# Optimization experiments

Measured on AMD Instinct MI355X. Metric: run time of the kernel, lower is better.

The kernel has to match this reference:

```python
import jax, jax.numpy as jnp
import numpy as np
import math

B, L, M = 8, 1024, 1024
H, D, DK, DFF = 16, 1024, 64, 4096
EPS = 1e-5


def _ln(x, g, b):
    mu = jnp.mean(x, axis=-1, keepdims=True)
    var = jnp.mean((x - mu) ** 2, axis=-1, keepdims=True)
    return (x - mu) * jax.lax.rsqrt(var + EPS) * g + b


def _mha(x, kv, Wq, bq, Wk, bk, Wv, bv, Wo, bo, masked):
    # x: [B,Lq,D], kv: [B,Lk,D]; per-head weights stacked: Wq [H,D,DK], bq [H,DK]
    Q = jnp.einsum('bld,hdk->bhlk', x, Wq) + bq[None, :, None, :]
    K = jnp.einsum('bld,hdk->bhlk', kv, Wk) + bk[None, :, None, :]
    V = jnp.einsum('bld,hdk->bhlk', kv, Wv) + bv[None, :, None, :]
    scores = jnp.einsum('bhqk,bhmk->bhqm', Q, K) / math.sqrt(DK)
    p = jax.nn.softmax(scores, axis=-1)
    if masked:
        # faithful to source: mask applied AFTER softmax (multiply by tril ones)
        Lq = x.shape[1]
        tril = jnp.tril(jnp.ones((Lq, kv.shape[1]), dtype=p.dtype))
        p = p * tril
    z = jnp.einsum('bhqm,bhmk->bhqk', p, V)  # [B,H,Lq,DK]
    z = jnp.transpose(z, (0, 2, 1, 3)).reshape(x.shape[0], x.shape[1], H * DK)
    return z @ Wo + bo


def _forward(x, enc, Wq1, bq1, Wk1, bk1, Wv1, bv1, Wo1, bo1,
             Wq2, bq2, Wk2, bk2, Wv2, bv2, Wo2, bo2,
             W1, b1, W2, b2, g1, be1, g2, be2, g3, be3):
    z = _mha(x, x, Wq1, bq1, Wk1, bk1, Wv1, bv1, Wo1, bo1, masked=True)
    x = _ln(z + x, g1, be1)
    z = _mha(x, enc, Wq2, bq2, Wk2, bk2, Wv2, bv2, Wo2, bo2, masked=False)
    x = _ln(z + x, g2, be2)
    # Conv1d(k=1) pair == per-token MLP: relu(x @ W1 + b1) @ W2 + b2
    y = jax.nn.relu(x @ W1 + b1) @ W2 + b2
    return _ln(y + x, g3, be3)


def setup_inputs() -> dict:
    key = jax.random.key(0)
    ks = jax.random.split(key, 16)
    s = 0.02
    return {
        'x': jax.random.normal(ks[0], (B, L, D), jnp.float32),
        'enc': jax.random.normal(ks[1], (B, M, D), jnp.float32),
        'Wq1': jax.random.normal(ks[2], (H, D, DK), jnp.float32) * s,
        'bq1': jnp.zeros((H, DK), jnp.float32),
        'Wk1': jax.random.normal(ks[3], (H, D, DK), jnp.float32) * s,
        'bk1': jnp.zeros((H, DK), jnp.float32),
        'Wv1': jax.random.normal(ks[4], (H, D, DK), jnp.float32) * s,
        'bv1': jnp.zeros((H, DK), jnp.float32),
        'Wo1': jax.random.normal(ks[5], (H * DK, D), jnp.float32) * s,
        'bo1': jnp.zeros((D,), jnp.float32),
        'Wq2': jax.random.normal(ks[6], (H, D, DK), jnp.float32) * s,
        'bq2': jnp.zeros((H, DK), jnp.float32),
        'Wk2': jax.random.normal(ks[7], (H, D, DK), jnp.float32) * s,
        'bk2': jnp.zeros((H, DK), jnp.float32),
        'Wv2': jax.random.normal(ks[8], (H, D, DK), jnp.float32) * s,
        'bv2': jnp.zeros((H, DK), jnp.float32),
        'Wo2': jax.random.normal(ks[9], (H * DK, D), jnp.float32) * s,
        'bo2': jnp.zeros((D,), jnp.float32),
        'W1': jax.random.normal(ks[10], (D, DFF), jnp.float32) * s,
        'b1': jnp.zeros((DFF,), jnp.float32),
        'W2': jax.random.normal(ks[11], (DFF, D), jnp.float32) * s,
        'b2': jnp.zeros((D,), jnp.float32),
        'g1': jnp.ones((D,), jnp.float32), 'be1': jnp.zeros((D,), jnp.float32),
        'g2': jnp.ones((D,), jnp.float32), 'be2': jnp.zeros((D,), jnp.float32),
        'g3': jnp.ones((D,), jnp.float32), 'be3': jnp.zeros((D,), jnp.float32),
    }


def reference(x, enc, Wq1, bq1, Wk1, bk1, Wv1, bv1, Wo1, bo1,
              Wq2, bq2, Wk2, bk2, Wv2, bv2, Wo2, bo2,
              W1, b1, W2, b2, g1, be1, g2, be2, g3, be3):
    return _forward(x, enc, Wq1, bq1, Wk1, bk1, Wv1, bv1, Wo1, bo1,
                    Wq2, bq2, Wk2, bk2, Wv2, bv2, Wo2, bo2,
                    W1, b1, W2, b2, g1, be1, g2, be2, g3, be3)
```

## Files before the change

kernel.cpp:

```cpp
#include <hip/hip_runtime.h>
#include <hip/hip_bf16.h>

typedef __bf16 bf16;
typedef __bf16 bf16x8 __attribute__((ext_vector_type(8)));
typedef __bf16 bf16x4v __attribute__((ext_vector_type(4)));
typedef float f32x4 __attribute__((ext_vector_type(4)));

#define DEV static __device__ __forceinline__

DEV void gll16(const void* g, void* l) {
  __builtin_amdgcn_global_load_lds((__attribute__((address_space(1))) void*)g,
                                   (__attribute__((address_space(3))) void*)l,
                                   16, 0, 0);
}

DEV bf16 tobf(float f) { return (bf16)f; }

__global__ void cast_f2b_kernel(const float* __restrict__ in, bf16* __restrict__ out, int n4) {
  int i = blockIdx.x * 256 + threadIdx.x;
  if (i < n4) {
    const float4 v = ((const float4*)in)[i];
    bf16x4v o;
    o[0] = tobf(v.x); o[1] = tobf(v.y); o[2] = tobf(v.z); o[3] = tobf(v.w);
    ((bf16x4v*)out)[i] = o;
  }
}

__global__ __launch_bounds__(256)
void tpack_kernel(const float* __restrict__ in, bf16* __restrict__ out,
                  int K, int N, int in_hs, int out_hs, float scale) {
  __shared__ float tile[32][33];
  const int k0 = blockIdx.x << 5, n0 = blockIdx.y << 5;
  const float* ip = in + (size_t)blockIdx.z * in_hs;
  bf16* op = out + (size_t)blockIdx.z * out_hs;
  const int tx = threadIdx.x & 31, ty = threadIdx.x >> 5;
#pragma unroll
  for (int r = 0; r < 4; ++r)
    tile[ty * 4 + r][tx] = ip[(size_t)(k0 + ty * 4 + r) * N + n0 + tx];
  __syncthreads();
#pragma unroll
  for (int r = 0; r < 4; ++r)
    op[(size_t)(n0 + ty * 4 + r) * K + k0 + tx] = tobf(tile[tx][ty * 4 + r] * scale);
}

__global__ void bscale_kernel(const float* __restrict__ in, float* __restrict__ out, int n, float s) {
  int i = blockIdx.x * 256 + threadIdx.x;
  if (i < n) out[i] = in[i] * s;
}

template<int EPI>
__global__ __launch_bounds__(256, 2)
void gemm_bt(const bf16* __restrict__ A, const bf16* __restrict__ W,
             const float* __restrict__ bias, const float* __restrict__ resid,
             void* __restrict__ outv, int M, int N, int K) {
  __shared__ bf16 sA[2][128 * 64];
  __shared__ bf16 sB[2][128 * 64];
  const int nbx = N >> 7;
  const int nwg = (M >> 7) * nbx;
  int bid = (int)blockIdx.x;
  bid = (bid & 7) * (nwg >> 3) + (bid >> 3);
  const int tm = bid / nbx, tn = bid - tm * nbx;
  const int tid = threadIdx.x;
  const int lane = tid & 63;
  const int w = tid >> 6;
  const int wm = (w >> 1) << 6, wn = (w & 1) << 6;
  const int l15 = lane & 15, l4 = lane >> 4;

  int srow[4], scol[4];
#pragma unroll
  for (int j = 0; j < 4; ++j) {
    int g = tid + (j << 8);
    srow[j] = g >> 3;
    scol[j] = ((g & 7) ^ (srow[j] & 7)) << 3;
  }
  const bf16* Abase = A + (size_t)(tm * 128) * K;
  const bf16* Bbase = W + (size_t)(tn * 128) * K;

  f32x4 acc[4][4] = {};
  const int nt = K >> 6;
  int cur = 0;

  auto stage = [&](int buf, int t) {
    const int kb = t << 6;
#pragma unroll
    for (int j = 0; j < 4; ++j) {
      int g = tid + (j << 8);
      gll16(Abase + (size_t)srow[j] * K + kb + scol[j], &sA[buf][g << 3]);
    }
#pragma unroll
    for (int j = 0; j < 4; ++j) {
      int g = tid + (j << 8);
      gll16(Bbase + (size_t)srow[j] * K + kb + scol[j], &sB[buf][g << 3]);
    }
  };

  stage(0, 0);
  __syncthreads();

  for (int t = 0; t < nt; ++t) {
    if (t + 1 < nt) stage(cur ^ 1, t + 1);
    bf16x8 af[4][2], bfm[4][2];
#pragma unroll
    for (int mi = 0; mi < 4; ++mi)
#pragma unroll
      for (int kk = 0; kk < 2; ++kk) {
        int r = wm + (mi << 4) + l15;
        int off = (r << 7) + (kk << 6) + (l4 << 4);
        off ^= (r & 7) << 4;
        af[mi][kk] = *(const bf16x8*)((const char*)sA[cur] + off);
      }
#pragma unroll
    for (int ni = 0; ni < 4; ++ni)
#pragma unroll
      for (int kk = 0; kk < 2; ++kk) {
        int r = wn + (ni << 4) + l15;
        int off = (r << 7) + (kk << 6) + (l4 << 4);
        off ^= (r & 7) << 4;
        bfm[ni][kk] = *(const bf16x8*)((const char*)sB[cur] + off);
      }
#pragma unroll
    for (int mi = 0; mi < 4; ++mi)
#pragma unroll
      for (int ni = 0; ni < 4; ++ni)
#pragma unroll
        for (int kk = 0; kk < 2; ++kk)
          acc[mi][ni] = __builtin_amdgcn_mfma_f32_16x16x32_bf16(af[mi][kk], bfm[ni][kk],
                                                                acc[mi][ni], 0, 0, 0);
    __syncthreads();
    cur ^= 1;
  }

  const int row0 = tm * 128 + wm + (l4 << 2);
  const int col0 = tn * 128 + wn + l15;
#pragma unroll
  for (int ni = 0; ni < 4; ++ni) {
    const int col = col0 + (ni << 4);
    const float bv = bias ? bias[col] : 0.f;
#pragma unroll
    for (int mi = 0; mi < 4; ++mi) {
      const int rr = row0 + (mi << 4);
      f32x4 v = acc[mi][ni];
      if (EPI == 0) {
        bf16* out = (bf16*)outv;
#pragma unroll
        for (int r = 0; r < 4; ++r) out[(size_t)(rr + r) * N + col] = tobf(v[r] + bv);
      } else if (EPI == 1) {
        float* out = (float*)outv;
#pragma unroll
        for (int r = 0; r < 4; ++r) {
          size_t idx = (size_t)(rr + r) * N + col;
          out[idx] = v[r] + bv + resid[idx];
        }
      } else if (EPI == 2) {
        bf16* out = (bf16*)outv;
#pragma unroll
        for (int r = 0; r < 4; ++r) out[(size_t)(rr + r) * N + col] = tobf(fmaxf(v[r] + bv, 0.f));
      } else {
        bf16* out = (bf16*)outv;
        const int bb = rr >> 10, l0 = rr & 1023;
        const int hh = col >> 6, dk = col & 63;
        bf16x4v pk;
#pragma unroll
        for (int r = 0; r < 4; ++r) pk[r] = tobf(v[r] + bv);
        *(bf16x4v*)(out + ((size_t)((bb * 16 + hh) * 64 + dk) << 10) + l0) = pk;
      }
    }
  }
}

template<bool MASKED>
__global__ __launch_bounds__(256, 3)
void attn_kernel(const bf16* __restrict__ Qp, const bf16* __restrict__ Kp,
                 const bf16* __restrict__ Vt, bf16* __restrict__ Z) {
  __shared__ bf16 sK[2][64 * 64];
  __shared__ bf16 sV[2][64 * 64];
  __shared__ bf16 sP[4][32 * 72];
  const int Lk = 1024;
  const int d = blockIdx.x;
  const int bh = d & 127, qb = d >> 7;
  const int b = bh >> 4, h = bh & 15;
  const int q0 = qb << 7;
  const int tid = threadIdx.x, lane = tid & 63, w = tid >> 6;
  const int l15 = lane & 15, l4 = lane >> 4;

  const bf16* Qb = Qp + ((size_t)(b * 1024 + q0 + w * 32)) * 1024 + h * 64;
  bf16x8 qf[2][2];
#pragma unroll
  for (int mi = 0; mi < 2; ++mi)
#pragma unroll
    for (int kk = 0; kk < 2; ++kk)
      qf[mi][kk] = *(const bf16x8*)(Qb + (size_t)((mi << 4) + l15) * 1024 + (kk << 5) + (l4 << 3));

  f32x4 o[4][2] = {};
  float Mr[2][4], Lr[2][4];
#pragma unroll
  for (int mi = 0; mi < 2; ++mi)
#pragma unroll
    for (int r = 0; r < 4; ++r) { Mr[mi][r] = -1e30f; Lr[mi][r] = 0.f; }

  const bf16* Kb = Kp + ((size_t)b * Lk) * 1024 + h * 64;
  const bf16* Vb = Vt + ((size_t)(b * 16 + h)) * 64 * Lk;

  auto stage = [&](int buf, int t, bool withV) {
    const int kv0 = t << 6;
#pragma unroll
    for (int j = 0; j < 2; ++j) {
      int g = tid + (j << 8);
      int r = g >> 3;
      int sc = ((g & 7) ^ (r & 7)) << 3;
      gll16(Kb + (size_t)(kv0 + r) * 1024 + sc, &sK[buf][g << 3]);
      if (withV) gll16(Vb + (size_t)r * Lk + kv0 + sc, &sV[buf][g << 3]);
    }
  };
  auto needPV = [&](int t) -> bool { return !MASKED || ((t << 6) < q0 + 128); };

  const int NT = Lk >> 6;
  stage(0, 0, true);
  __syncthreads();
  int cur = 0;

  for (int t = 0; t < NT; ++t) {
    if (t + 1 < NT) stage(cur ^ 1, t + 1, needPV(t + 1));
    const int kv0 = t << 6;

    bf16x8 kf[4][2];
#pragma unroll
    for (int n = 0; n < 4; ++n)
#pragma unroll
      for (int kk = 0; kk < 2; ++kk) {
        int r = (n << 4) + l15;
        int off = (r << 7) + (kk << 6) + (l4 << 4);
        off ^= (r & 7) << 4;
        kf[n][kk] = *(const bf16x8*)((const char*)sK[cur] + off);
      }
    f32x4 s[4][2] = {};
#pragma unroll
    for (int n = 0; n < 4; ++n)
#pragma unroll
      for (int mi = 0; mi < 2; ++mi)
#pragma unroll
        for (int kk = 0; kk < 2; ++kk)
          s[n][mi] = __builtin_amdgcn_mfma_f32_16x16x32_bf16(qf[mi][kk], kf[n][kk],
                                                             s[n][mi], 0, 0, 0);

#pragma unroll
    for (int mi = 0; mi < 2; ++mi)
#pragma unroll
      for (int r = 0; r < 4; ++r) {
        float tmx = fmaxf(fmaxf(s[0][mi][r], s[1][mi][r]), fmaxf(s[2][mi][r], s[3][mi][r]));
#pragma unroll
        for (int dd = 1; dd < 16; dd <<= 1) tmx = fmaxf(tmx, __shfl_xor(tmx, dd, 64));
        const float Mn = fmaxf(Mr[mi][r], tmx);
        const float al = __expf(Mr[mi][r] - Mn);
        float rs = 0.f;
#pragma unroll
        for (int n = 0; n < 4; ++n) {
          float p = __expf(s[n][mi][r] - Mn);
          s[n][mi][r] = p;
          rs += p;
        }
#pragma unroll
        for (int dd = 1; dd < 16; dd <<= 1) rs += __shfl_xor(rs, dd, 64);
        Lr[mi][r] = Lr[mi][r] * al + rs;
        Mr[mi][r] = Mn;
#pragma unroll
        for (int nd = 0; nd < 4; ++nd) o[nd][mi][r] *= al;
      }

    if (needPV(t)) {
#pragma unroll
      for (int n = 0; n < 4; ++n)
#pragma unroll
        for (int mi = 0; mi < 2; ++mi)
#pragma unroll
          for (int r = 0; r < 4; ++r) {
            float v = s[n][mi][r];
            if (MASKED) {
              int cg = kv0 + (n << 4) + l15;
              int rg = q0 + (w << 5) + (mi << 4) + (l4 << 2) + r;
              if (cg > rg) v = 0.f;
            }
            sP[w][((mi << 4) + (l4 << 2) + r) * 72 + (n << 4) + l15] = tobf(v);
          }

      bf16x8 vf[4][2], pa[2][2];
#pragma unroll
      for (int nd = 0; nd < 4; ++nd)
#pragma unroll
        for (int kk = 0; kk < 2; ++kk) {
          int r = (nd << 4) + l15;
          int off = (r << 7) + (kk << 6) + (l4 << 4);
          off ^= (r & 7) << 4;
          vf[nd][kk] = *(const bf16x8*)((const char*)sV[cur] + off);
        }
#pragma unroll
      for (int mi = 0; mi < 2; ++mi)
#pragma unroll
        for (int kk = 0; kk < 2; ++kk)
          pa[mi][kk] = *(const bf16x8*)((const char*)sP[w] +
                                        ((mi << 4) + l15) * 144 + (kk << 6) + (l4 << 4));
#pragma unroll
      for (int nd = 0; nd < 4; ++nd)
#pragma unroll
        for (int mi = 0; mi < 2; ++mi)
#pragma unroll
          for (int kk = 0; kk < 2; ++kk)
            o[nd][mi] = __builtin_amdgcn_mfma_f32_16x16x32_bf16(pa[mi][kk], vf[nd][kk],
                                                                o[nd][mi], 0, 0, 0);
    }
    __syncthreads();
    cur ^= 1;
  }

  float inv[2][4];
#pragma unroll
  for (int mi = 0; mi < 2; ++mi)
#pragma unroll
    for (int r = 0; r < 4; ++r) inv[mi][r] = 1.f / Lr[mi][r];
  bf16* Zb = Z + ((size_t)(b * 1024 + q0 + w * 32)) * 1024 + h * 64;
#pragma unroll
  for (int nd = 0; nd < 4; ++nd)
#pragma unroll
    for (int mi = 0; mi < 2; ++mi)
#pragma unroll
      for (int r = 0; r < 4; ++r)
        Zb[(size_t)((mi << 4) + (l4 << 2) + r) * 1024 + (nd << 4) + l15] =
            tobf(o[nd][mi][r] * inv[mi][r]);
}

__global__ __launch_bounds__(256)
void ln_kernel(const float* __restrict__ in, const float* __restrict__ gw,
               const float* __restrict__ bw, float* __restrict__ outf,
               bf16* __restrict__ outb) {
  const int row = blockIdx.x, tid = threadIdx.x;
  const size_t base = (size_t)row << 10;
  const float4 v = *(const float4*)(in + base + tid * 4);
  float s = v.x + v.y + v.z + v.w;
  float ss = v.x * v.x + v.y * v.y + v.z * v.z + v.w * v.w;
#pragma unroll
  for (int d = 1; d < 64; d <<= 1) { s += __shfl_xor(s, d, 64); ss += __shfl_xor(ss, d, 64); }
  __shared__ float red[8];
  const int w = tid >> 6;
  if ((tid & 63) == 0) { red[w] = s; red[4 + w] = ss; }
  __syncthreads();
  s = red[0] + red[1] + red[2] + red[3];
  ss = red[4] + red[5] + red[6] + red[7];
  const float mu = s * (1.f / 1024.f);
  const float var = ss * (1.f / 1024.f) - mu * mu;
  const float rstd = rsqrtf(var + 1e-5f);
  const float4 g4 = *(const float4*)(gw + tid * 4);
  const float4 b4 = *(const float4*)(bw + tid * 4);
  const float o0 = (v.x - mu) * rstd * g4.x + b4.x;
  const float o1 = (v.y - mu) * rstd * g4.y + b4.y;
  const float o2 = (v.z - mu) * rstd * g4.z + b4.z;
  const float o3 = (v.w - mu) * rstd * g4.w + b4.w;
  if (outf) { float4 of; of.x = o0; of.y = o1; of.z = o2; of.w = o3;
              *(float4*)(outf + base + tid * 4) = of; }
  if (outb) { bf16x4v ob; ob[0] = tobf(o0); ob[1] = tobf(o1); ob[2] = tobf(o2); ob[3] = tobf(o3);
              *(bf16x4v*)(outb + base + tid * 4) = ob; }
}

extern "C" void kernel_launch(void* const* d_in, const int* in_sizes, int n_in,
                              void* d_out, int out_size, void* d_ws, size_t ws_size,
                              hipStream_t stream) {
  const float* x   = (const float*)d_in[0];
  const float* enc = (const float*)d_in[1];
  const float* Wq1 = (const float*)d_in[2];
  const float* bq1 = (const float*)d_in[3];
  const float* Wk1 = (const float*)d_in[4];
  const float* bk1 = (const float*)d_in[5];
  const float* Wv1 = (const float*)d_in[6];
  const float* bv1 = (const float*)d_in[7];
  const float* Wo1 = (const float*)d_in[8];
  const float* bo1 = (const float*)d_in[9];
  const float* Wq2 = (const float*)d_in[10];
  const float* bq2 = (const float*)d_in[11];
  const float* Wk2 = (const float*)d_in[12];
  const float* bk2 = (const float*)d_in[13];
  const float* Wv2 = (const float*)d_in[14];
  const float* bv2 = (const float*)d_in[15];
  const float* Wo2 = (const float*)d_in[16];
  const float* bo2 = (const float*)d_in[17];
  const float* W1  = (const float*)d_in[18];
  const float* b1  = (const float*)d_in[19];
  const float* W2  = (const float*)d_in[20];
  const float* b2  = (const float*)d_in[21];
  const float* g1  = (const float*)d_in[22];
  const float* be1 = (const float*)d_in[23];
  const float* g2  = (const float*)d_in[24];
  const float* be2 = (const float*)d_in[25];
  const float* g3  = (const float*)d_in[26];
  const float* be3 = (const float*)d_in[27];

  char* ws = (char*)d_ws;
  size_t off = 0;
  auto alloc = [&](size_t bytes) { char* p = ws + off; off += (bytes + 255) & ~(size_t)255; return p; };
  const size_t ACT = (size_t)8 * 1024 * 1024 * 2;
  const size_t WSQ = (size_t)1024 * 1024 * 2;

  bf16* xb    = (bf16*)alloc(ACT);
  bf16* encb  = (bf16*)alloc(ACT);
  bf16* Wq1t  = (bf16*)alloc(WSQ);
  bf16* Wk1t  = (bf16*)alloc(WSQ);
  bf16* Wv1t  = (bf16*)alloc(WSQ);
  bf16* Wq2t  = (bf16*)alloc(WSQ);
  bf16* Wk2t  = (bf16*)alloc(WSQ);
  bf16* Wv2t  = (bf16*)alloc(WSQ);
  bf16* Wo1t  = (bf16*)alloc(WSQ);
  bf16* Wo2t  = (bf16*)alloc(WSQ);
  bf16* W1t   = (bf16*)alloc((size_t)4096 * 1024 * 2);
  bf16* W2t   = (bf16*)alloc((size_t)4096 * 1024 * 2);
  float* sbq1 = (float*)alloc(4096);
  float* sbq2 = (float*)alloc(4096);
  char*  S    = alloc((size_t)64 * 1024 * 1024);
  float* rbuf = (float*)alloc((size_t)8 * 1024 * 1024 * 4);
  float* xnf  = (float*)alloc((size_t)8 * 1024 * 1024 * 4);
  bf16*  xnb  = (bf16*)alloc(ACT);

  bf16* q1   = (bf16*)(S);
  bf16* k1   = (bf16*)(S + ACT);
  bf16* vt1  = (bf16*)(S + 2 * ACT);
  bf16* z1   = (bf16*)(S + 3 * ACT);
  bf16* hbuf = (bf16*)S;

  dim3 b256(256);
  cast_f2b_kernel<<<8192, b256, 0, stream>>>(x, xb, 2097152);
  cast_f2b_kernel<<<8192, b256, 0, stream>>>(enc, encb, 2097152);
  tpack_kernel<<<dim3(32, 2, 16), b256, 0, stream>>>(Wq1, Wq1t, 1024, 64, 65536, 65536, 0.125f);
  tpack_kernel<<<dim3(32, 2, 16), b256, 0, stream>>>(Wk1, Wk1t, 1024, 64, 65536, 65536, 1.f);
  tpack_kernel<<<dim3(32, 2, 16), b256, 0, stream>>>(Wv1, Wv1t, 1024, 64, 65536, 65536, 1.f);
  tpack_kernel<<<dim3(32, 2, 16), b256, 0, stream>>>(Wq2, Wq2t, 1024, 64, 65536, 65536, 0.125f);
  tpack_kernel<<<dim3(32, 2, 16), b256, 0, stream>>>(Wk2, Wk2t, 1024, 64, 65536, 65536, 1.f);
  tpack_kernel<<<dim3(32, 2, 16), b256, 0, stream>>>(Wv2, Wv2t, 1024, 64, 65536, 65536, 1.f);
  tpack_kernel<<<dim3(32, 32, 1), b256, 0, stream>>>(Wo1, Wo1t, 1024, 1024, 0, 0, 1.f);
  tpack_kernel<<<dim3(32, 32, 1), b256, 0, stream>>>(Wo2, Wo2t, 1024, 1024, 0, 0, 1.f);
  tpack_kernel<<<dim3(32, 128, 1), b256, 0, stream>>>(W1, W1t, 1024, 4096, 0, 0, 1.f);
  tpack_kernel<<<dim3(128, 32, 1), b256, 0, stream>>>(W2, W2t, 4096, 1024, 0, 0, 1.f);
  bscale_kernel<<<4, b256, 0, stream>>>(bq1, sbq1, 1024, 0.125f);
  bscale_kernel<<<4, b256, 0, stream>>>(bq2, sbq2, 1024, 0.125f);

  gemm_bt<0><<<512, b256, 0, stream>>>(xb, Wq1t, sbq1, nullptr, q1, 8192, 1024, 1024);
  gemm_bt<0><<<512, b256, 0, stream>>>(xb, Wk1t, bk1, nullptr, k1, 8192, 1024, 1024);
  gemm_bt<3><<<512, b256, 0, stream>>>(xb, Wv1t, bv1, nullptr, vt1, 8192, 1024, 1024);
  attn_kernel<true><<<1024, b256, 0, stream>>>(q1, k1, vt1, z1);
  gemm_bt<1><<<512, b256, 0, stream>>>(z1, Wo1t, bo1, x, rbuf, 8192, 1024, 1024);
  ln_kernel<<<8192, b256, 0, stream>>>(rbuf, g1, be1, xnf, xnb);

  gemm_bt<0><<<512, b256, 0, stream>>>(xnb, Wq2t, sbq2, nullptr, q1, 8192, 1024, 1024);
  gemm_bt<0><<<512, b256, 0, stream>>>(encb, Wk2t, bk2, nullptr, k1, 8192, 1024, 1024);
  gemm_bt<3><<<512, b256, 0, stream>>>(encb, Wv2t, bv2, nullptr, vt1, 8192, 1024, 1024);
  attn_kernel<false><<<1024, b256, 0, stream>>>(q1, k1, vt1, z1);
  gemm_bt<1><<<512, b256, 0, stream>>>(z1, Wo2t, bo2, xnf, rbuf, 8192, 1024, 1024);
  ln_kernel<<<8192, b256, 0, stream>>>(rbuf, g2, be2, xnf, xnb);

  gemm_bt<2><<<2048, b256, 0, stream>>>(xnb, W1t, b1, nullptr, hbuf, 8192, 4096, 1024);
  gemm_bt<1><<<512, b256, 0, stream>>>(hbuf, W2t, b2, xnf, rbuf, 8192, 1024, 4096);
  ln_kernel<<<8192, b256, 0, stream>>>(rbuf, g3, be3, (float*)d_out, nullptr);
}
```

Measured before the change: 664.0 us.

## Compute transposed scores in attention and pass P via register shuffles

The attention kernel now computes S^T, with K as the A operand and Q as B, so that each lane holds the scores for one query row. The row max and sum then need only two cross-lane shuffles instead of four per value. The softmax probabilities are packed to bf16 with v_cvt_pk_bf16_f32 and moved into the PV MFMA operand layout with lane shuffles, which removes the per-wave LDS scratch buffer sP and its stores and loads. The exp becomes exp2 with log2(e) folded into the Q weight and bias scaling, the mask is applied only on tiles that need it, and launch bounds rise to 4 waves per SIMD. The gains could be offset by the added shuffles and by register pressure at the higher occupancy target.

```diff
diff --git a/kernel.cpp b/kernel.cpp
--- a/kernel.cpp
+++ b/kernel.cpp
@@ -5,6 +5,8 @@
 typedef __bf16 bf16x8 __attribute__((ext_vector_type(8)));
 typedef __bf16 bf16x4v __attribute__((ext_vector_type(4)));
 typedef float f32x4 __attribute__((ext_vector_type(4)));
+typedef unsigned int u32;
+typedef u32 u32x4 __attribute__((ext_vector_type(4)));
 
 #define DEV static __device__ __forceinline__
 
@@ -15,6 +17,12 @@
 }
 
 DEV bf16 tobf(float f) { return (bf16)f; }
+
+DEV u32 cvtpk(float lo, float hi) {
+  u32 r;
+  asm("v_cvt_pk_bf16_f32 %0, %1, %2" : "=v"(r) : "v"(lo), "v"(hi));
+  return r;
+}
 
 __global__ void cast_f2b_kernel(const float* __restrict__ in, bf16* __restrict__ out, int n4) {
   int i = blockIdx.x * 256 + threadIdx.x;
@@ -169,12 +177,11 @@
 }
 
 template<bool MASKED>
-__global__ __launch_bounds__(256, 3)
+__global__ __launch_bounds__(256, 4)
 void attn_kernel(const bf16* __restrict__ Qp, const bf16* __restrict__ Kp,
                  const bf16* __restrict__ Vt, bf16* __restrict__ Z) {
   __shared__ bf16 sK[2][64 * 64];
   __shared__ bf16 sV[2][64 * 64];
-  __shared__ bf16 sP[4][32 * 72];
   const int Lk = 1024;
   const int d = blockIdx.x;
   const int bh = d & 127, qb = d >> 7;
@@ -192,11 +199,7 @@
       qf[mi][kk] = *(const bf16x8*)(Qb + (size_t)((mi << 4) + l15) * 1024 + (kk << 5) + (l4 << 3));
 
   f32x4 o[4][2] = {};
-  float Mr[2][4], Lr[2][4];
-#pragma unroll
-  for (int mi = 0; mi < 2; ++mi)
-#pragma unroll
-    for (int r = 0; r < 4; ++r) { Mr[mi][r] = -1e30f; Lr[mi][r] = 0.f; }
+  float Mr[2] = {-1e30f, -1e30f}, Lr[2] = {0.f, 0.f};
 
   const bf16* Kb = Kp + ((size_t)b * Lk) * 1024 + h * 64;
   const bf16* Vb = Vt + ((size_t)(b * 16 + h)) * 64 * Lk;
@@ -223,90 +226,113 @@
     if (t + 1 < NT) stage(cur ^ 1, t + 1, needPV(t + 1));
     const int kv0 = t << 6;
 
-    bf16x8 kf[4][2];
-#pragma unroll
-    for (int n = 0; n < 4; ++n)
+    f32x4 s[4][2] = {};
+#pragma unroll
+    for (int n = 0; n < 4; ++n) {
+      bf16x8 kf[2];
 #pragma unroll
       for (int kk = 0; kk < 2; ++kk) {
         int r = (n << 4) + l15;
         int off = (r << 7) + (kk << 6) + (l4 << 4);
         off ^= (r & 7) << 4;
-        kf[n][kk] = *(const bf16x8*)((const char*)sK[cur] + off);
-      }
-    f32x4 s[4][2] = {};
-#pragma unroll
-    for (int n = 0; n < 4; ++n)
+        kf[kk] = *(const bf16x8*)((const char*)sK[cur] + off);
+      }
 #pragma unroll
       for (int mi = 0; mi < 2; ++mi)
 #pragma unroll
         for (int kk = 0; kk < 2; ++kk)
-          s[n][mi] = __builtin_amdgcn_mfma_f32_16x16x32_bf16(qf[mi][kk], kf[n][kk],
+          s[n][mi] = __builtin_amdgcn_mfma_f32_16x16x32_bf16(kf[kk], qf[mi][kk],
                                                              s[n][mi], 0, 0, 0);
-
-#pragma unroll
-    for (int mi = 0; mi < 2; ++mi)
-#pragma unroll
-      for (int r = 0; r < 4; ++r) {
-        float tmx = fmaxf(fmaxf(s[0][mi][r], s[1][mi][r]), fmaxf(s[2][mi][r], s[3][mi][r]));
-#pragma unroll
-        for (int dd = 1; dd < 16; dd <<= 1) tmx = fmaxf(tmx, __shfl_xor(tmx, dd, 64));
-        const float Mn = fmaxf(Mr[mi][r], tmx);
-        const float al = __expf(Mr[mi][r] - Mn);
-        float rs = 0.f;
-#pragma unroll
-        for (int n = 0; n < 4; ++n) {
-          float p = __expf(s[n][mi][r] - Mn);
+    }
+
+    float alv[2];
+#pragma unroll
+    for (int mi = 0; mi < 2; ++mi) {
+      float tmx = s[0][mi][0];
+#pragma unroll
+      for (int n = 0; n < 4; ++n)
+#pragma unroll
+        for (int r = 0; r < 4; ++r) tmx = fmaxf(tmx, s[n][mi][r]);
+      tmx = fmaxf(tmx, __shfl_xor(tmx, 16, 64));
+      tmx = fmaxf(tmx, __shfl_xor(tmx, 32, 64));
+      const float Mn = fmaxf(Mr[mi], tmx);
+      alv[mi] = exp2f(Mr[mi] - Mn);
+      float rs = 0.f;
+#pragma unroll
+      for (int n = 0; n < 4; ++n)
+#pragma unroll
+        for (int r = 0; r < 4; ++r) {
+          float p = exp2f(s[n][mi][r] - Mn);
           s[n][mi][r] = p;
           rs += p;
         }
-#pragma unroll
-        for (int dd = 1; dd < 16; dd <<= 1) rs += __shfl_xor(rs, dd, 64);
-        Lr[mi][r] = Lr[mi][r] * al + rs;
-        Mr[mi][r] = Mn;
-#pragma unroll
-        for (int nd = 0; nd < 4; ++nd) o[nd][mi][r] *= al;
+      rs += __shfl_xor(rs, 16, 64);
+      rs += __shfl_xor(rs, 32, 64);
+      Lr[mi] = Lr[mi] * alv[mi] + rs;
+      Mr[mi] = Mn;
+    }
+
+#pragma unroll
+    for (int mi = 0; mi < 2; ++mi)
+#pragma unroll
+      for (int r = 0; r < 4; ++r) {
+        float a = __shfl(alv[mi], (l4 << 2) + r, 64);
+#pragma unroll
+        for (int nd = 0; nd < 4; ++nd) o[nd][mi][r] *= a;
       }
 
     if (needPV(t)) {
-#pragma unroll
-      for (int n = 0; n < 4; ++n)
-#pragma unroll
-        for (int mi = 0; mi < 2; ++mi)
+      const bool needMask = MASKED && (kv0 + 63 > q0 + (w << 5));
+      bf16x8 pa[2][2];
+#pragma unroll
+      for (int mi = 0; mi < 2; ++mi) {
+        u32 D0[4], D1[4];
+        const int qg = q0 + (w << 5) + (mi << 4) + l15;
+#pragma unroll
+        for (int n = 0; n < 4; ++n) {
+          float pv[4];
 #pragma unroll
           for (int r = 0; r < 4; ++r) {
-            float v = s[n][mi][r];
-            if (MASKED) {
-              int cg = kv0 + (n << 4) + l15;
-              int rg = q0 + (w << 5) + (mi << 4) + (l4 << 2) + r;
-              if (cg > rg) v = 0.f;
+            float p = s[n][mi][r];
+            if (needMask) {
+              int cg = kv0 + (n << 4) + (l4 << 2) + r;
+              if (cg > qg) p = 0.f;
             }
-            sP[w][((mi << 4) + (l4 << 2) + r) * 72 + (n << 4) + l15] = tobf(v);
+            pv[r] = p;
           }
-
-      bf16x8 vf[4][2], pa[2][2];
-#pragma unroll
-      for (int nd = 0; nd < 4; ++nd)
+          D0[n] = cvtpk(pv[0], pv[1]);
+          D1[n] = cvtpk(pv[2], pv[3]);
+        }
+        const int src = l15 + ((lane & 16) << 1);
+#pragma unroll
+        for (int kk = 0; kk < 2; ++kk) {
+          u32 v0 = (lane & 32) ? D0[2 * kk + 1] : D0[2 * kk];
+          u32 v1 = (lane & 32) ? D1[2 * kk + 1] : D1[2 * kk];
+          u32x4 tw;
+          tw[0] = (u32)__shfl((int)v0, src, 64);
+          tw[1] = (u32)__shfl((int)v1, src, 64);
+          tw[2] = (u32)__shfl((int)v0, src + 16, 64);
+          tw[3] = (u32)__shfl((int)v1, src + 16, 64);
+          pa[mi][kk] = *(bf16x8*)&tw;
+        }
+      }
+#pragma unroll
+      for (int nd = 0; nd < 4; ++nd) {
+        bf16x8 vf[2];
 #pragma unroll
         for (int kk = 0; kk < 2; ++kk) {
           int r = (nd << 4) + l15;
           int off = (r << 7) + (kk << 6) + (l4 << 4);
           off ^= (r & 7) << 4;
-          vf[nd][kk] = *(const bf16x8*)((const char*)sV[cur] + off);
+          vf[kk] = *(const bf16x8*)((const char*)sV[cur] + off);
         }
 #pragma unroll
-      for (int mi = 0; mi < 2; ++mi)
-#pragma unroll
-        for (int kk = 0; kk < 2; ++kk)
-          pa[mi][kk] = *(const bf16x8*)((const char*)sP[w] +
-                                        ((mi << 4) + l15) * 144 + (kk << 6) + (l4 << 4));
-#pragma unroll
-      for (int nd = 0; nd < 4; ++nd)
-#pragma unroll
         for (int mi = 0; mi < 2; ++mi)
 #pragma unroll
           for (int kk = 0; kk < 2; ++kk)
-            o[nd][mi] = __builtin_amdgcn_mfma_f32_16x16x32_bf16(pa[mi][kk], vf[nd][kk],
+            o[nd][mi] = __builtin_amdgcn_mfma_f32_16x16x32_bf16(pa[mi][kk], vf[kk],
                                                                 o[nd][mi], 0, 0, 0);
+      }
     }
     __syncthreads();
     cur ^= 1;
@@ -314,9 +340,11 @@
 
   float inv[2][4];
 #pragma unroll
-  for (int mi = 0; mi < 2; ++mi)
-#pragma unroll
-    for (int r = 0; r < 4; ++r) inv[mi][r] = 1.f / Lr[mi][r];
+  for (int mi = 0; mi < 2; ++mi) {
+    float il = 1.f / Lr[mi];
+#pragma unroll
+    for (int r = 0; r < 4; ++r) inv[mi][r] = __shfl(il, (l4 << 2) + r, 64);
+  }
   bf16* Zb = Z + ((size_t)(b * 1024 + q0 + w * 32)) * 1024 + h * 64;
 #pragma unroll
   for (int nd = 0; nd < 4; ++nd)
@@ -397,6 +425,7 @@
   auto alloc = [&](size_t bytes) { char* p = ws + off; off += (bytes + 255) & ~(size_t)255; return p; };
   const size_t ACT = (size_t)8 * 1024 * 1024 * 2;
   const size_t WSQ = (size_t)1024 * 1024 * 2;
+  const float QSC = 0.125f * 1.44269504088896f;
 
   bf16* xb    = (bf16*)alloc(ACT);
   bf16* encb  = (bf16*)alloc(ACT);
@@ -426,18 +455,18 @@
   dim3 b256(256);
   cast_f2b_kernel<<<8192, b256, 0, stream>>>(x, xb, 2097152);
   cast_f2b_kernel<<<8192, b256, 0, stream>>>(enc, encb, 2097152);
-  tpack_kernel<<<dim3(32, 2, 16), b256, 0, stream>>>(Wq1, Wq1t, 1024, 64, 65536, 65536, 0.125f);
+  tpack_kernel<<<dim3(32, 2, 16), b256, 0, stream>>>(Wq1, Wq1t, 1024, 64, 65536, 65536, QSC);
   tpack_kernel<<<dim3(32, 2, 16), b256, 0, stream>>>(Wk1, Wk1t, 1024, 64, 65536, 65536, 1.f);
   tpack_kernel<<<dim3(32, 2, 16), b256, 0, stream>>>(Wv1, Wv1t, 1024, 64, 65536, 65536, 1.f);
-  tpack_kernel<<<dim3(32, 2, 16), b256, 0, stream>>>(Wq2, Wq2t, 1024, 64, 65536, 65536, 0.125f);
+  tpack_kernel<<<dim3(32, 2, 16), b256, 0, stream>>>(Wq2, Wq2t, 1024, 64, 65536, 65536, QSC);
   tpack_kernel<<<dim3(32, 2, 16), b256, 0, stream>>>(Wk2, Wk2t, 1024, 64, 65536, 65536, 1.f);
   tpack_kernel<<<dim3(32, 2, 16), b256, 0, stream>>>(Wv2, Wv2t, 1024, 64, 65536, 65536, 1.f);
   tpack_kernel<<<dim3(32, 32, 1), b256, 0, stream>>>(Wo1, Wo1t, 1024, 1024, 0, 0, 1.f);
   tpack_kernel<<<dim3(32, 32, 1), b256, 0, stream>>>(Wo2, Wo2t, 1024, 1024, 0, 0, 1.f);
   tpack_kernel<<<dim3(32, 128, 1), b256, 0, stream>>>(W1, W1t, 1024, 4096, 0, 0, 1.f);
   tpack_kernel<<<dim3(128, 32, 1), b256, 0, stream>>>(W2, W2t, 4096, 1024, 0, 0, 1.f);
-  bscale_kernel<<<4, b256, 0, stream>>>(bq1, sbq1, 1024, 0.125f);
-  bscale_kernel<<<4, b256, 0, stream>>>(bq2, sbq2, 1024, 0.125f);
+  bscale_kernel<<<4, b256, 0, stream>>>(bq1, sbq1, 1024, QSC);
+  bscale_kernel<<<4, b256, 0, stream>>>(bq2, sbq2, 1024, QSC);
 
   gemm_bt<0><<<512, b256, 0, stream>>>(xb, Wq1t, sbq1, nullptr, q1, 8192, 1024, 1024);
   gemm_bt<0><<<512, b256, 0, stream>>>(xb, Wk1t, bk1, nullptr, k1, 8192, 1024, 1024);
```

New measurement: 693.9 us. 4.5% more time.
